# Kernel tuning notes

Hardware: AMD Instinct MI355X
Metric: run time of the kernel (lower is better)

Reference implementation:

```python
import jax, jax.numpy as jnp
import numpy as np

NEG_SLOPE = 0.2  # PyG GATConv default negative_slope
BN_EPS = 1e-5


def gat_layer(x, src, dst, W, b, a_src, a_dst, heads, out_ch, concat):
    # x: [N, Fin]; W: [Fin, heads*out_ch]; a_src/a_dst: [heads, out_ch]
    N = x.shape[0]
    h = (x @ W).reshape(N, heads, out_ch)
    s = (h * a_src).sum(-1)            # [N, H]
    d = (h * a_dst).sum(-1)            # [N, H]
    e = jax.nn.leaky_relu(s[src] + d[dst], NEG_SLOPE)   # [E, H]
    # segment softmax over incoming edges of each destination node
    m = jax.ops.segment_max(e, dst, num_segments=N)
    ex = jnp.exp(e - m[dst])
    denom = jax.ops.segment_sum(ex, dst, num_segments=N)
    alpha = ex / (denom[dst] + 1e-16)                   # [E, H]
    out = jax.ops.segment_sum(alpha[:, :, None] * h[src], dst, num_segments=N)  # [N,H,C]
    out = out.reshape(N, heads * out_ch) if concat else out.mean(axis=1)
    return out + b


def batchnorm(x, gamma, beta):
    mu = x.mean(axis=0)
    var = x.var(axis=0)
    return gamma * (x - mu) * jax.lax.rsqrt(var + BN_EPS) + beta


def setup_inputs() -> dict:
    key = jax.random.key(0)
    ks = jax.random.split(key, 24)
    N, E, Fin, Hd, heads, C = 50000, 800000, 128, 64, 4, 2
    wdim = Hd * heads  # 256
    inp = {
        'x': jax.random.normal(ks[0], (N, Fin), jnp.float32),
        'edge_index': jax.random.randint(ks[1], (2, E), 0, N, jnp.int64),
    }
    def glorot(k, shape):
        fan = shape[0] + shape[-1]
        return jax.random.normal(k, shape, jnp.float32) * np.sqrt(2.0 / fan)
    # layer 0: Fin -> heads x Hd (concat)
    inp['W0'] = glorot(ks[2], (Fin, wdim)); inp['b0'] = jnp.zeros((wdim,), jnp.float32)
    inp['asrc0'] = glorot(ks[3], (heads, Hd)); inp['adst0'] = glorot(ks[4], (heads, Hd))
    inp['g0'] = jnp.ones((wdim,), jnp.float32); inp['be0'] = jnp.zeros((wdim,), jnp.float32)
    # layer 1: wdim -> heads x Hd (concat)
    inp['W1'] = glorot(ks[5], (wdim, wdim)); inp['b1'] = jnp.zeros((wdim,), jnp.float32)
    inp['asrc1'] = glorot(ks[6], (heads, Hd)); inp['adst1'] = glorot(ks[7], (heads, Hd))
    inp['g1'] = jnp.ones((wdim,), jnp.float32); inp['be1'] = jnp.zeros((wdim,), jnp.float32)
    # layer 2: wdim -> 1 head x Hd (no concat)
    inp['W2'] = glorot(ks[8], (wdim, Hd)); inp['b2'] = jnp.zeros((Hd,), jnp.float32)
    inp['asrc2'] = glorot(ks[9], (1, Hd)); inp['adst2'] = glorot(ks[10], (1, Hd))
    inp['g2'] = jnp.ones((Hd,), jnp.float32); inp['be2'] = jnp.zeros((Hd,), jnp.float32)
    # classifier: Linear(2*Hd, Hd) -> ReLU -> Linear(Hd, C)
    inp['Wc1'] = glorot(ks[11], (2 * Hd, Hd)); inp['bc1'] = jnp.zeros((Hd,), jnp.float32)
    inp['Wc2'] = glorot(ks[12], (Hd, C)); inp['bc2'] = jnp.zeros((C,), jnp.float32)
    return inp


def reference(x, edge_index, W0, b0, asrc0, adst0, g0, be0,
              W1, b1, asrc1, adst1, g1, be1,
              W2, b2, asrc2, adst2, g2, be2,
              Wc1, bc1, Wc2, bc2):
    N = x.shape[0]
    # add self-loops (PyG GATConv default)
    loops = jnp.arange(N, dtype=edge_index.dtype)
    src = jnp.concatenate([edge_index[0], loops])
    dst = jnp.concatenate([edge_index[1], loops])
    heads, Hd = asrc0.shape[0], asrc0.shape[1]

    h = gat_layer(x, src, dst, W0, b0, asrc0, adst0, heads, Hd, True)
    h = jax.nn.relu(batchnorm(h, g0, be0))
    h = gat_layer(h, src, dst, W1, b1, asrc1, adst1, heads, Hd, True)
    h = jax.nn.relu(batchnorm(h, g1, be1))
    h = gat_layer(h, src, dst, W2, b2, asrc2, adst2, 1, Hd, False)
    h = jax.nn.relu(batchnorm(h, g2, be2))

    pooled = jnp.concatenate([h.mean(axis=0, keepdims=True),
                              h.max(axis=0, keepdims=True)], axis=1)  # [1, 2*Hd]
    z = jax.nn.relu(pooled @ Wc1 + bc1)
    return z @ Wc2 + bc2  # [1, num_classes]
```

## Files before the change

### kernel.cpp

```cpp
#include <hip/hip_runtime.h>


typedef unsigned int uint;
typedef unsigned short ushort;

#define NEG_SLOPE 0.2f
#define BN_EPS 1e-5f
#define NB_RED 256

__device__ __forceinline__ float bf2f(uint u) { return __uint_as_float(u << 16); }
__device__ __forceinline__ ushort f2bf(float f) {
    uint u = __float_as_uint(f);
    u += 0x7fff + ((u >> 16) & 1);
    return (ushort)(u >> 16);
}
__device__ __forceinline__ float lrelu(float x) { return x > 0.f ? x : NEG_SLOPE * x; }


__global__ void prep_kernel(const float* __restrict__ x, ushort* __restrict__ xb,
                            int total_real, int total_pad,
                            const float* __restrict__ W0, ushort* __restrict__ w0t,
                            const float* __restrict__ W1, ushort* __restrict__ w1t,
                            const float* __restrict__ W2, ushort* __restrict__ w2t,
                            const int* __restrict__ ei, int* __restrict__ deg, int E) {
    int i = blockIdx.x * blockDim.x + threadIdx.x;
    if (i < total_pad) {
        xb[i] = (i < total_real) ? f2bf(x[i]) : (ushort)0;
        return;
    }
    int j = i - total_pad;
    if (j < 32768) {
        int n = j / 128, k = j - n * 128;
        w0t[j] = f2bf(W0[(size_t)k * 256 + n]);
        return;
    }
    j -= 32768;
    if (j < 65536) {
        int n = j / 256, k = j - n * 256;
        w1t[j] = f2bf(W1[(size_t)k * 256 + n]);
        return;
    }
    j -= 65536;
    if (j < 16384) {
        int n = j / 256, k = j - n * 256;
        w2t[j] = f2bf(W2[(size_t)k * 64 + n]);
        return;
    }
    j -= 16384;
    if (j < E) atomicAdd(&deg[ei[E + j]], 1);
}


__global__ void scan_part(const int* __restrict__ deg, int* __restrict__ offsets,
                          int* __restrict__ bsum, int N) {
    __shared__ int sh[256];
    int t = threadIdx.x;
    int base = blockIdx.x * 1024 + t * 4;
    int v0 = (base + 0 < N) ? deg[base + 0] : 0;
    int v1 = (base + 1 < N) ? deg[base + 1] : 0;
    int v2 = (base + 2 < N) ? deg[base + 2] : 0;
    int v3 = (base + 3 < N) ? deg[base + 3] : 0;
    int s = v0 + v1 + v2 + v3;
    sh[t] = s;
    __syncthreads();
    for (int off = 1; off < 256; off <<= 1) {
        int y = (t >= off) ? sh[t - off] : 0;
        __syncthreads();
        sh[t] += y;
        __syncthreads();
    }
    int p = sh[t] - s;
    if (base + 0 < N) offsets[base + 0] = p;
    p += v0;
    if (base + 1 < N) offsets[base + 1] = p;
    p += v1;
    if (base + 2 < N) offsets[base + 2] = p;
    p += v2;
    if (base + 3 < N) offsets[base + 3] = p;
    if (t == 255) bsum[blockIdx.x] = sh[255];
}

__global__ void scan_top(const int* __restrict__ bsum, int* __restrict__ bexcl,
                         int nb, int* __restrict__ offsets, int N) {
    if (threadIdx.x == 0) {
        int run = 0;
        for (int b = 0; b < nb; ++b) { bexcl[b] = run; run += bsum[b]; }
        offsets[N] = run;
    }
}

__global__ void scan_add(int* __restrict__ offsets, int* __restrict__ cursor,
                         const int* __restrict__ bexcl, int N) {
    int add = bexcl[blockIdx.x];
    int base = blockIdx.x * 1024 + threadIdx.x * 4;
#pragma unroll
    for (int k = 0; k < 4; ++k) {
        int i = base + k;
        if (i < N) { int v = offsets[i] + add; offsets[i] = v; cursor[i] = v; }
    }
}

__global__ void scatter_kernel(const int* __restrict__ ei, int* __restrict__ cursor,
                               int* __restrict__ srcs, int E) {
    int e = blockIdx.x * blockDim.x + threadIdx.x;
    if (e < E) {
        int s = ei[e];
        int d = ei[E + e];
        int p = atomicAdd(&cursor[d], 1);
        srcs[p] = s;
    }
}


typedef __attribute__((ext_vector_type(8))) short bf16x8;
typedef __attribute__((ext_vector_type(4))) float floatx4;

template <int BN, int H>
__launch_bounds__(256)
__global__ void mfma_gemm_bt(const ushort* __restrict__ A, const ushort* __restrict__ Bt,
                             ushort* __restrict__ C, const float* __restrict__ asrc,
                             const float* __restrict__ adst, float* __restrict__ sv,
                             float* __restrict__ dv, int K, int Nn) {
    constexpr int WCOLS = (BN == 128) ? 2 : 1;
    constexpr int WROWS = 4 / WCOLS;
    constexpr int MT = 128 / (WROWS * 16);
    constexpr int NT = BN / (WCOLS * 16);
    constexpr int BCALLS = (BN * 32 * 2) / 4096;

    __shared__ ushort As[128 * 32];
    __shared__ ushort Bs[BN * 32];

    int t = threadIdx.x;
    int w = t >> 6, l = t & 63;
    int row0 = blockIdx.x * 128;
    int col0 = blockIdx.y * BN;
    int wr = (w / WCOLS) * (MT * 16);
    int wc = (w % WCOLS) * (NT * 16);

    floatx4 acc[MT][NT];
#pragma unroll
    for (int mi = 0; mi < MT; ++mi)
#pragma unroll
        for (int ni = 0; ni < NT; ++ni)
#pragma unroll
            for (int r = 0; r < 4; ++r) acc[mi][ni][r] = 0.f;

    int mrow = l & 15;
    int kc = (l >> 4) * 8;

    for (int kt = 0; kt < K; kt += 32) {
#pragma unroll
        for (int c = 0; c < 2; ++c) {
            int idx = c * 256 + t;
            const ushort* gp = A + (size_t)(row0 + (idx >> 2)) * K + kt + (idx & 3) * 8;
            __builtin_amdgcn_global_load_lds(
                (const __attribute__((address_space(1))) void*)gp,
                (__attribute__((address_space(3))) void*)(As + (idx & ~63) * 8),
                16, 0, 0);
        }
#pragma unroll
        for (int c = 0; c < BCALLS; ++c) {
            int idx = c * 256 + t;
            const ushort* gp = Bt + (size_t)(col0 + (idx >> 2)) * K + kt + (idx & 3) * 8;
            __builtin_amdgcn_global_load_lds(
                (const __attribute__((address_space(1))) void*)gp,
                (__attribute__((address_space(3))) void*)(Bs + (idx & ~63) * 8),
                16, 0, 0);
        }
        __syncthreads();

        bf16x8 af[MT], bfr[NT];
#pragma unroll
        for (int mi = 0; mi < MT; ++mi)
            af[mi] = *(const bf16x8*)&As[(wr + mi * 16 + mrow) * 32 + kc];
#pragma unroll
        for (int ni = 0; ni < NT; ++ni)
            bfr[ni] = *(const bf16x8*)&Bs[(wc + ni * 16 + mrow) * 32 + kc];
#pragma unroll
        for (int mi = 0; mi < MT; ++mi)
#pragma unroll
            for (int ni = 0; ni < NT; ++ni)
                acc[mi][ni] = __builtin_amdgcn_mfma_f32_16x16x32_bf16(
                    af[mi], bfr[ni], acc[mi][ni], 0, 0, 0);
        __syncthreads();
    }

#pragma unroll
    for (int mi = 0; mi < MT; ++mi) {
        int rbase = row0 + wr + mi * 16 + (l >> 4) * 4;
#pragma unroll
        for (int ni = 0; ni < NT; ++ni) {
            int col = col0 + wc + ni * 16 + (l & 15);
#pragma unroll
            for (int r = 0; r < 4; ++r)
                C[(size_t)(rbase + r) * Nn + col] = f2bf(acc[mi][ni][r]);
        }
    }

    float av[NT], bv[NT];
#pragma unroll
    for (int ni = 0; ni < NT; ++ni) {
        int ch = col0 + wc + ni * 16 + (l & 15);
        av[ni] = asrc[ch];
        bv[ni] = adst[ch];
    }
    int gh = (col0 + wc) >> 6;
#pragma unroll
    for (int mi = 0; mi < MT; ++mi) {
#pragma unroll
        for (int r = 0; r < 4; ++r) {
            float s = 0.f, d = 0.f;
#pragma unroll
            for (int ni = 0; ni < NT; ++ni) {
                float hv = acc[mi][ni][r];
                s += hv * av[ni];
                d += hv * bv[ni];
            }
#pragma unroll
            for (int m = 8; m >= 1; m >>= 1) {
                s += __shfl_xor(s, m);
                d += __shfl_xor(d, m);
            }
            if ((l & 15) == 0) {
                int row = row0 + wr + mi * 16 + (l >> 4) * 4 + r;
                sv[row * H + gh] = s;
                dv[row * H + gh] = d;
            }
        }
    }
}


__launch_bounds__(128)
__global__ void agg4_kernel(const ushort* __restrict__ hb, const float* __restrict__ sv,
                            const float* __restrict__ dv, const int* __restrict__ offsets,
                            const int* __restrict__ srcs, const float* __restrict__ bias,
                            ushort* __restrict__ zb, int N) {
    __shared__ float lsum[4][256];
    __shared__ float lden[4][4];

    int i = blockIdx.x;
    int t = threadIdx.x;
    int grp = t >> 5, gl = t & 31;
    int head = gl >> 3;
    int beg = offsets[i], end = offsets[i + 1];

    float d_i = dv[i * 4 + head];
    float ax[8] = {};
    float den = 0.f;

    int j = beg + grp;
    int srcn = (j < end) ? srcs[j] : 0;
    while (j < end) {
        float sval = sv[srcn * 4 + head];
        uint4 q = *(const uint4*)&hb[(size_t)srcn * 256 + gl * 8];
        int jn = j + 4;
        int srcn_n = (jn < end) ? srcs[jn] : 0;
        float wgt = __expf(fminf(lrelu(sval + d_i), 60.f));
        den += wgt;
        uint pr[4] = {q.x, q.y, q.z, q.w};
#pragma unroll
        for (int k = 0; k < 4; ++k) {
            ax[2 * k]     += wgt * bf2f(pr[k] & 0xffffu);
            ax[2 * k + 1] += wgt * bf2f(pr[k] >> 16);
        }
        j = jn; srcn = srcn_n;
    }

#pragma unroll
    for (int k = 0; k < 8; ++k) lsum[grp][gl * 8 + k] = ax[k];
    if ((gl & 7) == 0) lden[grp][head] = den;
    __syncthreads();

    int h = t >> 5;
    float wself = __expf(fminf(lrelu(sv[i * 4 + h] + dv[i * 4 + h]), 60.f));
    float dtot = lden[0][h] + lden[1][h] + lden[2][h] + lden[3][h] + wself + 1e-16f;
    float rden = 1.f / dtot;
    uint p = *(const uint*)&hb[(size_t)i * 256 + 2 * t];
    float a0 = lsum[0][2 * t] + lsum[1][2 * t] + lsum[2][2 * t] + lsum[3][2 * t]
             + wself * bf2f(p & 0xffffu);
    float a1 = lsum[0][2 * t + 1] + lsum[1][2 * t + 1] + lsum[2][2 * t + 1]
             + lsum[3][2 * t + 1] + wself * bf2f(p >> 16);
    a0 = a0 * rden + bias[2 * t];
    a1 = a1 * rden + bias[2 * t + 1];
    *(uint*)&zb[(size_t)i * 256 + 2 * t] = (uint)f2bf(a0) | ((uint)f2bf(a1) << 16);
}


__launch_bounds__(64)
__global__ void agg1_kernel(const ushort* __restrict__ hb, const float* __restrict__ sv,
                            const float* __restrict__ dv, const int* __restrict__ offsets,
                            const int* __restrict__ srcs, const float* __restrict__ bias,
                            ushort* __restrict__ zb, int N) {
    int i = blockIdx.x;
    int l = threadIdx.x;
    int grp = l >> 4, gl = l & 15;
    int beg = offsets[i], end = offsets[i + 1];

    float d_i = dv[i];
    float ax[4] = {};
    float den = 0.f;

    int j = beg + grp;
    int srcn = (j < end) ? srcs[j] : 0;
    while (j < end) {
        float sval = sv[srcn];
        uint2 q = *(const uint2*)&hb[(size_t)srcn * 64 + gl * 4];
        int jn = j + 4;
        int srcn_n = (jn < end) ? srcs[jn] : 0;
        float wgt = __expf(fminf(lrelu(sval + d_i), 60.f));
        den += wgt;
        ax[0] += wgt * bf2f(q.x & 0xffffu);
        ax[1] += wgt * bf2f(q.x >> 16);
        ax[2] += wgt * bf2f(q.y & 0xffffu);
        ax[3] += wgt * bf2f(q.y >> 16);
        j = jn; srcn = srcn_n;
    }

#pragma unroll
    for (int k = 0; k < 4; ++k) {
        ax[k] += __shfl_xor(ax[k], 16);
        ax[k] += __shfl_xor(ax[k], 32);
    }
    den += __shfl_xor(den, 16);
    den += __shfl_xor(den, 32);

    if (l < 16) {
        float wself = __expf(fminf(lrelu(sv[i] + d_i), 60.f));
        float rden = 1.f / (den + wself + 1e-16f);
        uint2 q = *(const uint2*)&hb[(size_t)i * 64 + gl * 4];
        float a0 = (ax[0] + wself * bf2f(q.x & 0xffffu)) * rden + bias[gl * 4 + 0];
        float a1 = (ax[1] + wself * bf2f(q.x >> 16)) * rden + bias[gl * 4 + 1];
        float a2 = (ax[2] + wself * bf2f(q.y & 0xffffu)) * rden + bias[gl * 4 + 2];
        float a3 = (ax[3] + wself * bf2f(q.y >> 16)) * rden + bias[gl * 4 + 3];
        uint2 o;
        o.x = (uint)f2bf(a0) | ((uint)f2bf(a1) << 16);
        o.y = (uint)f2bf(a2) | ((uint)f2bf(a3) << 16);
        *(uint2*)&zb[(size_t)i * 64 + gl * 4] = o;
    }
}


template <int F>
__launch_bounds__(256)
__global__ void bn_stats_kernel(const ushort* __restrict__ x, float* __restrict__ ps,
                                float* __restrict__ pq, int N) {
    constexpr int OCT = F / 8;
    __shared__ float lds_s[F], lds_q[F];
    int t = threadIdx.x;
    if (t < F) { lds_s[t] = 0.f; lds_q[t] = 0.f; }
    __syncthreads();

    float s[8] = {}, q[8] = {};
    int total8 = N * F / 8;
    for (int idx = blockIdx.x * 256 + t; idx < total8; idx += NB_RED * 256) {
        uint4 v = ((const uint4*)x)[idx];
        uint pr[4] = {v.x, v.y, v.z, v.w};
#pragma unroll
        for (int k = 0; k < 4; ++k) {
            float a = bf2f(pr[k] & 0xffffu);
            float b = bf2f(pr[k] >> 16);
            s[2 * k] += a;     q[2 * k] += a * a;
            s[2 * k + 1] += b; q[2 * k + 1] += b * b;
        }
    }
    int co = t % OCT;
#pragma unroll
    for (int j = 0; j < 8; ++j) {
        atomicAdd(&lds_s[co * 8 + j], s[j]);
        atomicAdd(&lds_q[co * 8 + j], q[j]);
    }
    __syncthreads();
    if (t < F) {
        ps[blockIdx.x * F + t] = lds_s[t];
        pq[blockIdx.x * F + t] = lds_q[t];
    }
}

__global__ void bn_final_kernel(const float* __restrict__ ps, const float* __restrict__ pq,
                                const float* __restrict__ g, const float* __restrict__ be,
                                float* __restrict__ scale, float* __restrict__ shift,
                                int N, int F) {
    int t = threadIdx.x;
    if (t < F) {
        float s = 0.f, q = 0.f;
        for (int b = 0; b < NB_RED; ++b) { s += ps[b * F + t]; q += pq[b * F + t]; }
        float mean = s / (float)N;
        float var = q / (float)N - mean * mean;
        float sc = g[t] * rsqrtf(var + BN_EPS);
        scale[t] = sc;
        shift[t] = be[t] - sc * mean;
    }
}

__global__ void bn_apply_kernel(uint* __restrict__ x, const float* __restrict__ scale,
                                const float* __restrict__ shift, int totalPairs, int Fmask) {
    int i = blockIdx.x * blockDim.x + threadIdx.x;
    if (i < totalPairs) {
        uint p = x[i];
        int c0 = (2 * i) & Fmask;
        float v0 = fmaxf(bf2f(p & 0xffffu) * scale[c0] + shift[c0], 0.f);
        float v1 = fmaxf(bf2f(p >> 16) * scale[c0 + 1] + shift[c0 + 1], 0.f);
        x[i] = (uint)f2bf(v0) | ((uint)f2bf(v1) << 16);
    }
}


__launch_bounds__(256)
__global__ void pool_kernel(const ushort* __restrict__ y, const float* __restrict__ scale,
                            const float* __restrict__ shift, float* __restrict__ psum,
                            float* __restrict__ pmax, int N) {
    constexpr int F = 64, OCT = 8;
    __shared__ float lds_s[F];
    __shared__ uint lds_m[F];
    int t = threadIdx.x;
    if (t < F) { lds_s[t] = 0.f; lds_m[t] = 0u; }
    __syncthreads();

    int co = t % OCT;
    float sc[8], sh[8];
#pragma unroll
    for (int j = 0; j < 8; ++j) { sc[j] = scale[co * 8 + j]; sh[j] = shift[co * 8 + j]; }

    float s[8] = {}, m[8] = {};
    int total8 = N * F / 8;
    for (int idx = blockIdx.x * 256 + t; idx < total8; idx += NB_RED * 256) {
        uint4 v = ((const uint4*)y)[idx];
        uint pr[4] = {v.x, v.y, v.z, v.w};
#pragma unroll
        for (int k = 0; k < 4; ++k) {
            float a = fmaxf(bf2f(pr[k] & 0xffffu) * sc[2 * k] + sh[2 * k], 0.f);
            float b = fmaxf(bf2f(pr[k] >> 16) * sc[2 * k + 1] + sh[2 * k + 1], 0.f);
            s[2 * k] += a;     m[2 * k] = fmaxf(m[2 * k], a);
            s[2 * k + 1] += b; m[2 * k + 1] = fmaxf(m[2 * k + 1], b);
        }
    }
#pragma unroll
    for (int j = 0; j < 8; ++j) {
        atomicAdd(&lds_s[co * 8 + j], s[j]);
        atomicMax(&lds_m[co * 8 + j], __float_as_uint(m[j]));
    }
    __syncthreads();
    if (t < F) {
        psum[blockIdx.x * F + t] = lds_s[t];
        pmax[blockIdx.x * F + t] = __uint_as_float(lds_m[t]);
    }
}

__global__ void classify_kernel(const float* __restrict__ psum, const float* __restrict__ pmax,
                                const float* __restrict__ Wc1, const float* __restrict__ bc1,
                                const float* __restrict__ Wc2, const float* __restrict__ bc2,
                                float* __restrict__ out, int N) {
    __shared__ float pooled[128];
    __shared__ float z[64];
    int t = threadIdx.x;
    if (t < 64) {
        float s = 0.f;
        for (int b = 0; b < NB_RED; ++b) s += psum[b * 64 + t];
        pooled[t] = s / (float)N;
    } else {
        int c = t - 64;
        float m = 0.f;
        for (int b = 0; b < NB_RED; ++b) m = fmaxf(m, pmax[b * 64 + c]);
        pooled[t] = m;
    }
    __syncthreads();
    if (t < 64) {
        float a = bc1[t];
        for (int k = 0; k < 128; ++k) a += pooled[k] * Wc1[k * 64 + t];
        z[t] = a > 0.f ? a : 0.f;
    }
    __syncthreads();
    if (t < 2) {
        float a = bc2[t];
        for (int j = 0; j < 64; ++j) a += z[j] * Wc2[j * 2 + t];
        out[t] = a;
    }
}


extern "C" void kernel_launch(void* const* d_in, const int* in_sizes, int n_in,
                              void* d_out, int out_size, void* d_ws, size_t ws_size,
                              hipStream_t stream) {
    const float* x   = (const float*)d_in[0];
    const int*   ei  = (const int*)d_in[1];
    const float* W0  = (const float*)d_in[2];  const float* b0  = (const float*)d_in[3];
    const float* as0 = (const float*)d_in[4];  const float* ad0 = (const float*)d_in[5];
    const float* g0  = (const float*)d_in[6];  const float* be0 = (const float*)d_in[7];
    const float* W1  = (const float*)d_in[8];  const float* b1  = (const float*)d_in[9];
    const float* as1 = (const float*)d_in[10]; const float* ad1 = (const float*)d_in[11];
    const float* g1  = (const float*)d_in[12]; const float* be1 = (const float*)d_in[13];
    const float* W2  = (const float*)d_in[14]; const float* b2  = (const float*)d_in[15];
    const float* as2 = (const float*)d_in[16]; const float* ad2 = (const float*)d_in[17];
    const float* g2  = (const float*)d_in[18]; const float* be2 = (const float*)d_in[19];
    const float* Wc1 = (const float*)d_in[20]; const float* bc1 = (const float*)d_in[21];
    const float* Wc2 = (const float*)d_in[22]; const float* bc2 = (const float*)d_in[23];
    float* out = (float*)d_out;

    const int N = in_sizes[0] / 128;
    const int E = in_sizes[1] / 2;
    const int Mpad = ((N + 127) / 128) * 128;
    const int NB_SCAN = (N + 1023) / 1024;

    char* ws = (char*)d_ws;
    size_t o = 0;
    auto alloc = [&](size_t bytes) -> void* {
        void* p = ws + o;
        o = (o + bytes + 255) & ~(size_t)255;
        return p;
    };
    int*    deg     = (int*)alloc((size_t)N * 4);
    int*    offsets = (int*)alloc((size_t)(N + 1) * 4);
    int*    cursor  = (int*)alloc((size_t)N * 4);
    int*    srcs    = (int*)alloc((size_t)E * 4);
    int*    bsum    = (int*)alloc((size_t)NB_SCAN * 4);
    int*    bexcl   = (int*)alloc((size_t)NB_SCAN * 4);
    ushort* xb      = (ushort*)alloc((size_t)Mpad * 128 * 2);
    ushort* w0t     = (ushort*)alloc((size_t)256 * 128 * 2);
    ushort* w1t     = (ushort*)alloc((size_t)256 * 256 * 2);
    ushort* w2t     = (ushort*)alloc((size_t)64 * 256 * 2);
    ushort* hb      = (ushort*)alloc((size_t)Mpad * 256 * 2);
    ushort* zb      = (ushort*)alloc((size_t)Mpad * 256 * 2);
    float*  sv      = (float*)alloc((size_t)Mpad * 4 * 4);
    float*  dv      = (float*)alloc((size_t)Mpad * 4 * 4);
    float*  ps      = (float*)alloc((size_t)NB_RED * 256 * 4);
    float*  pq      = (float*)alloc((size_t)NB_RED * 256 * 4);
    float*  scale   = (float*)alloc(256 * 4);
    float*  shift   = (float*)alloc(256 * 4);
    float*  psum    = (float*)alloc((size_t)NB_RED * 64 * 4);
    float*  pmax    = (float*)alloc((size_t)NB_RED * 64 * 4);

    hipMemsetAsync(deg, 0, (size_t)N * 4, stream);
    int prep_total = Mpad * 128 + 32768 + 65536 + 16384 + E;
    prep_kernel<<<(prep_total + 255) / 256, 256, 0, stream>>>(
        x, xb, N * 128, Mpad * 128, W0, w0t, W1, w1t, W2, w2t, ei, deg, E);

    scan_part<<<NB_SCAN, 256, 0, stream>>>(deg, offsets, bsum, N);
    scan_top<<<1, 64, 0, stream>>>(bsum, bexcl, NB_SCAN, offsets, N);
    scan_add<<<NB_SCAN, 256, 0, stream>>>(offsets, cursor, bexcl, N);
    scatter_kernel<<<(E + 255) / 256, 256, 0, stream>>>(ei, cursor, srcs, E);

    {
        dim3 gg(Mpad / 128, 2);
        mfma_gemm_bt<128, 4><<<gg, 256, 0, stream>>>(xb, w0t, hb, as0, ad0, sv, dv, 128, 256);
        agg4_kernel<<<N, 128, 0, stream>>>(hb, sv, dv, offsets, srcs, b0, zb, N);
        bn_stats_kernel<256><<<NB_RED, 256, 0, stream>>>(zb, ps, pq, N);
        bn_final_kernel<<<1, 256, 0, stream>>>(ps, pq, g0, be0, scale, shift, N, 256);
        bn_apply_kernel<<<(N * 128 + 255) / 256, 256, 0, stream>>>((uint*)zb, scale, shift,
                                                                   N * 128, 255);
    }
    {
        dim3 gg(Mpad / 128, 2);
        mfma_gemm_bt<128, 4><<<gg, 256, 0, stream>>>(zb, w1t, hb, as1, ad1, sv, dv, 256, 256);
        agg4_kernel<<<N, 128, 0, stream>>>(hb, sv, dv, offsets, srcs, b1, zb, N);
        bn_stats_kernel<256><<<NB_RED, 256, 0, stream>>>(zb, ps, pq, N);
        bn_final_kernel<<<1, 256, 0, stream>>>(ps, pq, g1, be1, scale, shift, N, 256);
        bn_apply_kernel<<<(N * 128 + 255) / 256, 256, 0, stream>>>((uint*)zb, scale, shift,
                                                                   N * 128, 255);
    }
    {
        dim3 gg(Mpad / 128, 1);
        mfma_gemm_bt<64, 1><<<gg, 256, 0, stream>>>(zb, w2t, hb, as2, ad2, sv, dv, 256, 64);
        agg1_kernel<<<N, 64, 0, stream>>>(hb, sv, dv, offsets, srcs, b2, zb, N);
        bn_stats_kernel<64><<<NB_RED, 256, 0, stream>>>(zb, ps, pq, N);
        bn_final_kernel<<<1, 64, 0, stream>>>(ps, pq, g2, be2, scale, shift, N, 64);
    }

    pool_kernel<<<NB_RED, 256, 0, stream>>>(zb, scale, shift, psum, pmax, N);
    classify_kernel<<<1, 128, 0, stream>>>(psum, pmax, Wc1, bc1, Wc2, bc2, out, N);
}
```

Measured before the change: 584.2 us.

## Split GAT aggregation per head and map heads to XCDs; fuse scan top into add

The 4-head aggregation kernel becomes one 64-thread block per (node, head), and the block index is decoded so each head's blocks go to a fixed pair of XCDs under round-robin dispatch. The aim is that each XCD's L2 only holds its head's 128-byte slice of the gathered feature rows, which should improve cache hit rates for the random source gathers. Cross-lane reduction now uses shuffles instead of shared memory and a barrier. The separate single-thread scan_top kernel is removed, and each scan_add block sums the preceding block totals itself, saving one launch. The cost is four times as many blocks, each node's edge list and sv values read once per head, and the XCD mapping assumes the hardware's round-robin dispatch order.

```diff
diff --git a/kernel.cpp b/kernel.cpp
--- a/kernel.cpp
+++ b/kernel.cpp
@@ -80,18 +80,22 @@
     if (t == 255) bsum[blockIdx.x] = sh[255];
 }
 
-__global__ void scan_top(const int* __restrict__ bsum, int* __restrict__ bexcl,
-                         int nb, int* __restrict__ offsets, int N) {
+__global__ void scan_add(int* __restrict__ offsets, int* __restrict__ cursor,
+                         const int* __restrict__ bsum, int N) {
+    __shared__ int sadd;
+    int nb = gridDim.x;
     if (threadIdx.x == 0) {
         int run = 0;
-        for (int b = 0; b < nb; ++b) { bexcl[b] = run; run += bsum[b]; }
-        offsets[N] = run;
-    }
-}
-
-__global__ void scan_add(int* __restrict__ offsets, int* __restrict__ cursor,
-                         const int* __restrict__ bexcl, int N) {
-    int add = bexcl[blockIdx.x];
+        for (int b = 0; b < (int)blockIdx.x; ++b) run += bsum[b];
+        sadd = run;
+        if ((int)blockIdx.x == nb - 1) {
+            int tot = run;
+            for (int b = blockIdx.x; b < nb; ++b) tot += bsum[b];
+            offsets[N] = tot;
+        }
+    }
+    __syncthreads();
+    int add = sadd;
     int base = blockIdx.x * 1024 + threadIdx.x * 4;
 #pragma unroll
     for (int k = 0; k < 4; ++k) {
@@ -231,59 +235,61 @@
 }
 
 
-__launch_bounds__(128)
+__launch_bounds__(64)
 __global__ void agg4_kernel(const ushort* __restrict__ hb, const float* __restrict__ sv,
                             const float* __restrict__ dv, const int* __restrict__ offsets,
                             const int* __restrict__ srcs, const float* __restrict__ bias,
                             ushort* __restrict__ zb, int N) {
-    __shared__ float lsum[4][256];
-    __shared__ float lden[4][4];
-
-    int i = blockIdx.x;
-    int t = threadIdx.x;
-    int grp = t >> 5, gl = t & 31;
-    int head = gl >> 3;
+    int b = blockIdx.x;
+    int xcd = b & 7;
+    int head = xcd >> 1;
+    int i = (b >> 3) * 2 + (xcd & 1);
+    if (i >= N) return;
+
+    int l = threadIdx.x;
+    int slot = l >> 3, lg = l & 7;
+    int cbase = head * 64 + lg * 8;
     int beg = offsets[i], end = offsets[i + 1];
-
     float d_i = dv[i * 4 + head];
-    float ax[8] = {};
+
+    float acc[8] = {};
     float den = 0.f;
-
-    int j = beg + grp;
-    int srcn = (j < end) ? srcs[j] : 0;
-    while (j < end) {
-        float sval = sv[srcn * 4 + head];
-        uint4 q = *(const uint4*)&hb[(size_t)srcn * 256 + gl * 8];
-        int jn = j + 4;
-        int srcn_n = (jn < end) ? srcs[jn] : 0;
-        float wgt = __expf(fminf(lrelu(sval + d_i), 60.f));
-        den += wgt;
+    for (int j = beg + slot; j < end; j += 8) {
+        int s0 = srcs[j];
+        float sval = sv[s0 * 4 + head];
+        uint4 q = *(const uint4*)&hb[(size_t)s0 * 256 + cbase];
+        float w = __expf(fminf(lrelu(sval + d_i), 60.f));
+        den += w;
         uint pr[4] = {q.x, q.y, q.z, q.w};
 #pragma unroll
         for (int k = 0; k < 4; ++k) {
-            ax[2 * k]     += wgt * bf2f(pr[k] & 0xffffu);
-            ax[2 * k + 1] += wgt * bf2f(pr[k] >> 16);
-        }
-        j = jn; srcn = srcn_n;
-    }
-
-#pragma unroll
-    for (int k = 0; k < 8; ++k) lsum[grp][gl * 8 + k] = ax[k];
-    if ((gl & 7) == 0) lden[grp][head] = den;
-    __syncthreads();
-
-    int h = t >> 5;
-    float wself = __expf(fminf(lrelu(sv[i * 4 + h] + dv[i * 4 + h]), 60.f));
-    float dtot = lden[0][h] + lden[1][h] + lden[2][h] + lden[3][h] + wself + 1e-16f;
-    float rden = 1.f / dtot;
-    uint p = *(const uint*)&hb[(size_t)i * 256 + 2 * t];
-    float a0 = lsum[0][2 * t] + lsum[1][2 * t] + lsum[2][2 * t] + lsum[3][2 * t]
-             + wself * bf2f(p & 0xffffu);
-    float a1 = lsum[0][2 * t + 1] + lsum[1][2 * t + 1] + lsum[2][2 * t + 1]
-             + lsum[3][2 * t + 1] + wself * bf2f(p >> 16);
-    a0 = a0 * rden + bias[2 * t];
-    a1 = a1 * rden + bias[2 * t + 1];
-    *(uint*)&zb[(size_t)i * 256 + 2 * t] = (uint)f2bf(a0) | ((uint)f2bf(a1) << 16);
+            acc[2 * k]     += w * bf2f(pr[k] & 0xffffu);
+            acc[2 * k + 1] += w * bf2f(pr[k] >> 16);
+        }
+    }
+#pragma unroll
+    for (int m = 8; m <= 32; m <<= 1) {
+        den += __shfl_xor(den, m);
+#pragma unroll
+        for (int k = 0; k < 8; ++k) acc[k] += __shfl_xor(acc[k], m);
+    }
+
+    if (slot == 0) {
+        float wself = __expf(fminf(lrelu(sv[i * 4 + head] + d_i), 60.f));
+        float rden = 1.f / (den + wself + 1e-16f);
+        uint4 qs = *(const uint4*)&hb[(size_t)i * 256 + cbase];
+        uint prs[4] = {qs.x, qs.y, qs.z, qs.w};
+        uint4 o;
+        uint ow[4];
+#pragma unroll
+        for (int k = 0; k < 4; ++k) {
+            float a0 = (acc[2 * k]     + wself * bf2f(prs[k] & 0xffffu)) * rden + bias[cbase + 2 * k];
+            float a1 = (acc[2 * k + 1] + wself * bf2f(prs[k] >> 16))     * rden + bias[cbase + 2 * k + 1];
+            ow[k] = (uint)f2bf(a0) | ((uint)f2bf(a1) << 16);
+        }
+        o.x = ow[0]; o.y = ow[1]; o.z = ow[2]; o.w = ow[3];
+        *(uint4*)&zb[(size_t)i * 256 + cbase] = o;
+    }
 }
 
 
@@ -501,6 +507,7 @@
     const int E = in_sizes[1] / 2;
     const int Mpad = ((N + 127) / 128) * 128;
     const int NB_SCAN = (N + 1023) / 1024;
+    const int agg4_grid = 8 * ((N + 1) / 2);
 
     char* ws = (char*)d_ws;
     size_t o = 0;
@@ -514,7 +521,6 @@
     int*    cursor  = (int*)alloc((size_t)N * 4);
     int*    srcs    = (int*)alloc((size_t)E * 4);
     int*    bsum    = (int*)alloc((size_t)NB_SCAN * 4);
-    int*    bexcl   = (int*)alloc((size_t)NB_SCAN * 4);
     ushort* xb      = (ushort*)alloc((size_t)Mpad * 128 * 2);
     ushort* w0t     = (ushort*)alloc((size_t)256 * 128 * 2);
     ushort* w1t     = (ushort*)alloc((size_t)256 * 256 * 2);
@@ -536,14 +542,13 @@
         x, xb, N * 128, Mpad * 128, W0, w0t, W1, w1t, W2, w2t, ei, deg, E);
 
     scan_part<<<NB_SCAN, 256, 0, stream>>>(deg, offsets, bsum, N);
-    scan_top<<<1, 64, 0, stream>>>(bsum, bexcl, NB_SCAN, offsets, N);
-    scan_add<<<NB_SCAN, 256, 0, stream>>>(offsets, cursor, bexcl, N);
+    scan_add<<<NB_SCAN, 256, 0, stream>>>(offsets, cursor, bsum, N);
     scatter_kernel<<<(E + 255) / 256, 256, 0, stream>>>(ei, cursor, srcs, E);
 
     {
         dim3 gg(Mpad / 128, 2);
         mfma_gemm_bt<128, 4><<<gg, 256, 0, stream>>>(xb, w0t, hb, as0, ad0, sv, dv, 128, 256);
-        agg4_kernel<<<N, 128, 0, stream>>>(hb, sv, dv, offsets, srcs, b0, zb, N);
+        agg4_kernel<<<agg4_grid, 64, 0, stream>>>(hb, sv, dv, offsets, srcs, b0, zb, N);
         bn_stats_kernel<256><<<NB_RED, 256, 0, stream>>>(zb, ps, pq, N);
         bn_final_kernel<<<1, 256, 0, stream>>>(ps, pq, g0, be0, scale, shift, N, 256);
         bn_apply_kernel<<<(N * 128 + 255) / 256, 256, 0, stream>>>((uint*)zb, scale, shift,
@@ -552,7 +557,7 @@
     {
         dim3 gg(Mpad / 128, 2);
         mfma_gemm_bt<128, 4><<<gg, 256, 0, stream>>>(zb, w1t, hb, as1, ad1, sv, dv, 256, 256);
-        agg4_kernel<<<N, 128, 0, stream>>>(hb, sv, dv, offsets, srcs, b1, zb, N);
+        agg4_kernel<<<agg4_grid, 64, 0, stream>>>(hb, sv, dv, offsets, srcs, b1, zb, N);
         bn_stats_kernel<256><<<NB_RED, 256, 0, stream>>>(zb, ps, pq, N);
         bn_final_kernel<<<1, 256, 0, stream>>>(ps, pq, g1, be1, scale, shift, N, 256);
         bn_apply_kernel<<<(N * 128 + 255) / 256, 256, 0, stream>>>((uint*)zb, scale, shift,
```

Measured after the change: 634.5 us. 1.09x slower.
